# Performance work log

Measured on AMD Instinct MI355X. Metric: run time of the kernel, lower is better.

Reference implementation:

```python
import jax, jax.numpy as jnp
import numpy as np

BIDAT = 4


def _biatt(atoms_vector, amino_vector, U, Wp2c, bp2c, Wc2p, bc2p,
           Whc, bhc, Whp, bhp, Wac, bac, Wap, bap, Wcc, bcc, Wcp, bcp):
    cfs, pfs = [], []
    for i in range(BIDAT):  # fixed small structural loop (4 distinct param sets)
        # bilinear tanh affinity: [Na, Np]
        A = jnp.tanh((atoms_vector @ U[i]) @ amino_vector.T)
        atoms_trans = A @ jnp.tanh(amino_vector @ Wp2c[i] + bp2c[i])      # [Na, D]
        amino_trans = A.T @ jnp.tanh(atoms_vector @ Wc2p[i] + bc2p[i])    # [Np, D]
        atoms_tmp = jnp.concatenate(
            [jnp.tanh(atoms_vector @ Whc[i] + bhc[i]), atoms_trans], axis=1)  # [Na, 2D]
        amino_tmp = jnp.concatenate(
            [jnp.tanh(amino_vector @ Whp[i] + bhp[i]), amino_trans], axis=1)  # [Np, 2D]
        # NOTE: softmax over axis=1 of a [N,1] tensor == all-ones (faithful to torch source)
        atoms_att = jax.nn.softmax(atoms_tmp @ Wac[i] + bac[i], axis=1)   # [Na, 1]
        amino_att = jax.nn.softmax(amino_tmp @ Wap[i] + bap[i], axis=1)   # [Np, 1]
        cfs.append(atoms_vector * atoms_att)
        pfs.append(amino_vector * amino_att)
    cf_final = jnp.concatenate(cfs, axis=1) @ Wcc + bcc   # [Na, D]
    pf_final = jnp.concatenate(pfs, axis=1) @ Wcp + bcp   # [Np, D]
    return cf_final, pf_final


def setup_inputs() -> dict:
    D, Na, Np = 512, 6144, 6144
    key = jax.random.key(0)
    ks = jax.random.split(key, 20)
    s = 0.04  # ~xavier-scale init for D=512
    return {
        "atoms_vector": jax.random.normal(ks[0], (Na, D), jnp.float32),
        "amino_vector": jax.random.normal(ks[1], (Np, D), jnp.float32),
        "U":    jax.random.normal(ks[2], (BIDAT, D, D), jnp.float32) * s,
        "Wp2c": jax.random.normal(ks[3], (BIDAT, D, D), jnp.float32) * s,
        "bp2c": jnp.zeros((BIDAT, D), jnp.float32),
        "Wc2p": jax.random.normal(ks[4], (BIDAT, D, D), jnp.float32) * s,
        "bc2p": jnp.zeros((BIDAT, D), jnp.float32),
        "Whc":  jax.random.normal(ks[5], (BIDAT, D, D), jnp.float32) * s,
        "bhc":  jnp.zeros((BIDAT, D), jnp.float32),
        "Whp":  jax.random.normal(ks[6], (BIDAT, D, D), jnp.float32) * s,
        "bhp":  jnp.zeros((BIDAT, D), jnp.float32),
        "Wac":  jax.random.normal(ks[7], (BIDAT, 2 * D, 1), jnp.float32) * s,
        "bac":  jnp.zeros((BIDAT, 1), jnp.float32),
        "Wap":  jax.random.normal(ks[8], (BIDAT, 2 * D, 1), jnp.float32) * s,
        "bap":  jnp.zeros((BIDAT, 1), jnp.float32),
        "Wcc":  jax.random.normal(ks[9], (BIDAT * D, D), jnp.float32) * s,
        "bcc":  jnp.zeros((D,), jnp.float32),
        "Wcp":  jax.random.normal(ks[10], (BIDAT * D, D), jnp.float32) * s,
        "bcp":  jnp.zeros((D,), jnp.float32),
    }


def reference(atoms_vector, amino_vector, U, Wp2c, bp2c, Wc2p, bc2p,
              Whc, bhc, Whp, bhp, Wac, bac, Wap, bap, Wcc, bcc, Wcp, bcp):
    return _biatt(atoms_vector, amino_vector, U, Wp2c, bp2c, Wc2p, bc2p,
                  Whc, bhc, Whp, bhp, Wac, bac, Wap, bap, Wcc, bcc, Wcp, bcp)
```

## Files before the change

### kernel.cpp

```cpp
#include <hip/hip_runtime.h>
#include <hip/hip_bf16.h>

#define DDIM 512
#define NROWS 6144
#define BM 64
#define BN 128
#define BK 32
#define KSTEPS (DDIM / BK)

typedef __attribute__((ext_vector_type(8))) short short8;
typedef __attribute__((ext_vector_type(4))) float f32x4;

#define GLDS16(g, s)                                          \
  __builtin_amdgcn_global_load_lds(                           \
      (const __attribute__((address_space(1))) void*)(g),     \
      (__attribute__((address_space(3))) void*)(s), 16, 0, 0)

__global__ __launch_bounds__(256) void prep_w(
    const float* __restrict__ Wcc, const float* __restrict__ Wcp,
    __hip_bfloat16* __restrict__ Wt) {
    const float* W = blockIdx.z ? Wcp : Wcc;
    unsigned short* o = (unsigned short*)Wt + (size_t)blockIdx.z * DDIM * DDIM;
    __shared__ float lds[32][33];
    const int k0 = blockIdx.x * 32, n0 = blockIdx.y * 32;
    #pragma unroll
    for (int e = 0; e < 4; ++e) {
        int idx = e * 256 + threadIdx.x;
        int kk = idx >> 5, nn = idx & 31;
        float s = 0.f;
        #pragma unroll
        for (int i = 0; i < 4; ++i)
            s += W[(size_t)(i * DDIM + k0 + kk) * DDIM + n0 + nn];
        lds[kk][nn] = s;
    }
    __syncthreads();
    #pragma unroll
    for (int e = 0; e < 4; ++e) {
        int idx = e * 256 + threadIdx.x;
        int nn = idx >> 5, kk = idx & 31;
        __hip_bfloat16 h = __float2bfloat16(lds[kk][nn]);
        o[(size_t)(n0 + nn) * DDIM + k0 + kk] = *(unsigned short*)&h;
    }
}

__global__ __launch_bounds__(256, 3) void gemm_bias(
    const float* __restrict__ Aat, const float* __restrict__ Aam,
    const __hip_bfloat16* __restrict__ Wtall,
    const float* __restrict__ bias0, const float* __restrict__ bias1,
    float* __restrict__ C) {
  __shared__ float As[2][BM * BK];
  __shared__ unsigned short Bs[2][BN * BK];

  const int z = blockIdx.z;
  const float* A = z ? Aam : Aat;
  const unsigned short* Wt = (const unsigned short*)Wtall + (size_t)z * DDIM * DDIM;
  const float* bias = z ? bias1 : bias0;
  float* Cz = C + (size_t)z * NROWS * DDIM;

  const int tid = threadIdx.x;
  const int w = tid >> 6, l = tid & 63;
  const int m0 = blockIdx.x * BM;
  const int n0 = blockIdx.y * BN;

  const float* srcA0;
  const float* srcA1;
  const unsigned short* srcB0;
  const unsigned short* srcB1;
  {
    int r0 = w * 16 + (l >> 3);
    int r1 = r0 + 8;
    srcA0 = A + (size_t)(m0 + r0) * DDIM + (((l & 7) ^ (r0 & 7)) << 2);
    srcA1 = A + (size_t)(m0 + r1) * DDIM + (((l & 7) ^ (r1 & 7)) << 2);
    int q0 = w * 32 + (l >> 2);
    int q1 = q0 + 16;
    srcB0 = Wt + (size_t)(n0 + q0) * DDIM + (((l & 3) ^ ((q0 >> 1) & 3)) << 3);
    srcB1 = Wt + (size_t)(n0 + q1) * DDIM + (((l & 3) ^ ((q1 >> 1) & 3)) << 3);
  }
  const unsigned ldsA0 = (w * 2 + 0) * 256, ldsA1 = (w * 2 + 1) * 256;
  const unsigned ldsB0 = (w * 2 + 0) * 512, ldsB1 = (w * 2 + 1) * 512;

#define STAGE(buf, kk)                                 \
  do {                                                 \
    GLDS16(srcA0 + (kk) * BK, &As[buf][ldsA0]);        \
    GLDS16(srcA1 + (kk) * BK, &As[buf][ldsA1]);        \
    GLDS16(srcB0 + (kk) * BK, &Bs[buf][ldsB0]);        \
    GLDS16(srcB1 + (kk) * BK, &Bs[buf][ldsB1]);        \
  } while (0)

  f32x4 acc[2][4];
  #pragma unroll
  for (int i = 0; i < 2; ++i)
    #pragma unroll
    for (int j = 0; j < 4; ++j) acc[i][j] = (f32x4){0.f, 0.f, 0.f, 0.f};

  const int s0 = (l >> 4) * 2;
  const int bs = (l >> 4);
  const int lr = l & 15;

#define COMPUTE(buf)                                                          \
  do {                                                                        \
    short8 afr[2];                                                            \
    _Pragma("unroll")                                                         \
    for (int tm = 0; tm < 2; ++tm) {                                          \
      int r = (w >> 1) * 32 + tm * 16 + lr;                                   \
      f32x4 x0 = *(const f32x4*)&As[buf][r * BK + (((s0 + 0) ^ (r & 7)) << 2)]; \
      f32x4 x1 = *(const f32x4*)&As[buf][r * BK + (((s0 + 1) ^ (r & 7)) << 2)]; \
      float xv[8] = {x0[0], x0[1], x0[2], x0[3], x1[0], x1[1], x1[2], x1[3]}; \
      _Pragma("unroll")                                                       \
      for (int e = 0; e < 8; ++e) {                                           \
        __hip_bfloat16 h = __float2bfloat16(xv[e]);                           \
        afr[tm][e] = *(short*)&h;                                             \
      }                                                                       \
    }                                                                         \
    _Pragma("unroll")                                                         \
    for (int tn = 0; tn < 4; ++tn) {                                          \
      int r = (w & 1) * 64 + tn * 16 + lr;                                    \
      short8 bf = *(const short8*)&Bs[buf][r * BK + ((bs ^ ((r >> 1) & 3)) << 3)]; \
      acc[0][tn] = __builtin_amdgcn_mfma_f32_16x16x32_bf16(afr[0], bf, acc[0][tn], 0, 0, 0); \
      acc[1][tn] = __builtin_amdgcn_mfma_f32_16x16x32_bf16(afr[1], bf, acc[1][tn], 0, 0, 0); \
    }                                                                         \
  } while (0)

  STAGE(0, 0);
  __syncthreads();

  for (int t = 0; t < KSTEPS; t += 2) {
    STAGE(1, t + 1);
    COMPUTE(0);
    __syncthreads();
    if (t + 2 < KSTEPS) STAGE(0, t + 2);
    COMPUTE(1);
    __syncthreads();
  }

  const int rg = (l >> 4) * 4;
  #pragma unroll
  for (int tn = 0; tn < 4; ++tn) {
    const int col = n0 + (w & 1) * 64 + tn * 16 + lr;
    const float bv = bias[col];
    #pragma unroll
    for (int tm = 0; tm < 2; ++tm) {
      const int row = m0 + (w >> 1) * 32 + tm * 16 + rg;
      #pragma unroll
      for (int r = 0; r < 4; ++r)
        Cz[(size_t)(row + r) * DDIM + col] = acc[tm][tn][r] + bv;
    }
  }
#undef STAGE
#undef COMPUTE
}

extern "C" void kernel_launch(void* const* d_in, const int* in_sizes, int n_in,
                              void* d_out, int out_size, void* d_ws, size_t ws_size,
                              hipStream_t stream) {
    const float* atoms = (const float*)d_in[0];
    const float* amino = (const float*)d_in[1];
    const float* Wcc   = (const float*)d_in[15];
    const float* bcc   = (const float*)d_in[16];
    const float* Wcp   = (const float*)d_in[17];
    const float* bcp   = (const float*)d_in[18];
    float* out = (float*)d_out;

    __hip_bfloat16* Wt = (__hip_bfloat16*)d_ws;

    dim3 fgrid(DDIM / 32, DDIM / 32, 2);
    prep_w<<<fgrid, 256, 0, stream>>>(Wcc, Wcp, Wt);

    dim3 ggrid(NROWS / BM, DDIM / BN, 2);
    gemm_bias<<<ggrid, 256, 0, stream>>>(atoms, amino, Wt, bcc, bcp, out);
}
```

Before: 138.4 us.

## Triple-buffer GEMM loads with vmcnt waits and vectorize weight prep

The GEMM main loop moves from double buffering with two __syncthreads per pair of k-steps to a three-stage LDS ring. Loads are issued two steps ahead, and each step uses an explicit s_waitcnt vmcnt plus a single s_barrier, which lets global-to-LDS copies overlap more with MFMA compute. The weight-fold prep kernel now uses float4 loads and ushort4 stores over 32x64 tiles to cut instruction count. LDS use grows by 50%, which may reduce occupancy at 3 blocks per CU, and the correctness of the manual vmcnt accounting depends on each stage issuing exactly four loads per thread.

```diff
diff --git a/kernel.cpp b/kernel.cpp
--- a/kernel.cpp
+++ b/kernel.cpp
@@ -21,25 +21,35 @@
     __hip_bfloat16* __restrict__ Wt) {
     const float* W = blockIdx.z ? Wcp : Wcc;
     unsigned short* o = (unsigned short*)Wt + (size_t)blockIdx.z * DDIM * DDIM;
-    __shared__ float lds[32][33];
-    const int k0 = blockIdx.x * 32, n0 = blockIdx.y * 32;
+    __shared__ float lds[32][65];
+    const int k0 = blockIdx.x * 32, n0 = blockIdx.y * 64;
     #pragma unroll
-    for (int e = 0; e < 4; ++e) {
-        int idx = e * 256 + threadIdx.x;
-        int kk = idx >> 5, nn = idx & 31;
-        float s = 0.f;
+    for (int u = 0; u < 2; ++u) {
+        int idx = u * 256 + threadIdx.x;
+        int kk = idx >> 4, c = idx & 15;
+        float4 s = {0.f, 0.f, 0.f, 0.f};
         #pragma unroll
-        for (int i = 0; i < 4; ++i)
-            s += W[(size_t)(i * DDIM + k0 + kk) * DDIM + n0 + nn];
-        lds[kk][nn] = s;
+        for (int i = 0; i < 4; ++i) {
+            float4 v = *(const float4*)&W[(size_t)(i * DDIM + k0 + kk) * DDIM + n0 + c * 4];
+            s.x += v.x; s.y += v.y; s.z += v.z; s.w += v.w;
+        }
+        lds[kk][c * 4 + 0] = s.x;
+        lds[kk][c * 4 + 1] = s.y;
+        lds[kk][c * 4 + 2] = s.z;
+        lds[kk][c * 4 + 3] = s.w;
     }
     __syncthreads();
     #pragma unroll
-    for (int e = 0; e < 4; ++e) {
-        int idx = e * 256 + threadIdx.x;
-        int nn = idx >> 5, kk = idx & 31;
-        __hip_bfloat16 h = __float2bfloat16(lds[kk][nn]);
-        o[(size_t)(n0 + nn) * DDIM + k0 + kk] = *(unsigned short*)&h;
+    for (int u = 0; u < 2; ++u) {
+        int idx = u * 256 + threadIdx.x;
+        int nr = idx >> 3, kc = idx & 7;
+        ushort4 p;
+        #pragma unroll
+        for (int j = 0; j < 4; ++j) {
+            __hip_bfloat16 h = __float2bfloat16(lds[kc * 4 + j][nr]);
+            ((unsigned short*)&p)[j] = *(unsigned short*)&h;
+        }
+        *(ushort4*)&o[(size_t)(n0 + nr) * DDIM + k0 + kc * 4] = p;
     }
 }
 
@@ -48,8 +58,8 @@
     const __hip_bfloat16* __restrict__ Wtall,
     const float* __restrict__ bias0, const float* __restrict__ bias1,
     float* __restrict__ C) {
-  __shared__ float As[2][BM * BK];
-  __shared__ unsigned short Bs[2][BN * BK];
+  __shared__ float As[3][BM * BK];
+  __shared__ unsigned short Bs[3][BN * BK];
 
   const int z = blockIdx.z;
   const float* A = z ? Aam : Aat;
@@ -122,15 +132,17 @@
   } while (0)
 
   STAGE(0, 0);
-  __syncthreads();
+  STAGE(1, 1);
 
-  for (int t = 0; t < KSTEPS; t += 2) {
-    STAGE(1, t + 1);
-    COMPUTE(0);
-    __syncthreads();
-    if (t + 2 < KSTEPS) STAGE(0, t + 2);
-    COMPUTE(1);
-    __syncthreads();
+  #pragma unroll
+  for (int t = 0; t < KSTEPS; ++t) {
+    if (t < KSTEPS - 1)
+      asm volatile("s_waitcnt vmcnt(4)" ::: "memory");
+    else
+      asm volatile("s_waitcnt vmcnt(0)" ::: "memory");
+    __builtin_amdgcn_s_barrier();
+    if (t + 2 < KSTEPS) STAGE((t + 2) % 3, t + 2);
+    COMPUTE(t % 3);
   }
 
   const int rg = (l >> 4) * 4;
@@ -163,7 +175,7 @@
 
     __hip_bfloat16* Wt = (__hip_bfloat16*)d_ws;
 
-    dim3 fgrid(DDIM / 32, DDIM / 32, 2);
+    dim3 fgrid(DDIM / 32, DDIM / 64, 2);
     prep_w<<<fgrid, 256, 0, stream>>>(Wcc, Wcp, Wt);
 
     dim3 ggrid(NROWS / BM, DDIM / BN, 2);
```

Result: faster. 134.1 us, median of 2 (-3.1%).
